# Kernel optimization log

Hardware: AMD Instinct MI355X
Metric: run time of the kernel (lower is better)

The kernel has to match this reference:

```python
import jax, jax.numpy as jnp
import numpy as np

NUM_HEADS = 16
NUM_KV_HEADS = 4
HEAD_DIM = 128
HIDDEN = 2048
SEQ = 2048
BATCH = 2
Q_PER_GROUP = NUM_HEADS // NUM_KV_HEADS          # 4
GROUP_SIZE = (Q_PER_GROUP + 2) * HEAD_DIM        # 768
TOTAL_PROJ = NUM_KV_HEADS * GROUP_SIZE           # 3072


def setup_inputs() -> dict:
    key = jax.random.key(0)
    k1, k2, k3 = jax.random.split(key, 3)
    x = jax.random.normal(k1, (SEQ, BATCH, HIDDEN), dtype=jnp.float32)
    w_qkv = jax.random.normal(k2, (TOTAL_PROJ, HIDDEN), dtype=jnp.float32) * 0.02
    w_proj = jax.random.normal(k3, (HIDDEN, NUM_HEADS * HEAD_DIM), dtype=jnp.float32) * 0.02
    return {"x": x, "w_qkv": w_qkv, "w_proj": w_proj}


def reference(x, w_qkv, w_proj):
    s, b, _ = x.shape
    # fused QKV projection (GQA-packed layout: per kv-group [q...q, k, v])
    qkv = jnp.einsum('sbh,ph->sbp', x, w_qkv)                       # [s,b,3072]
    qkv = qkv.reshape(s, b, NUM_KV_HEADS, GROUP_SIZE)
    q = qkv[..., :Q_PER_GROUP * HEAD_DIM].reshape(s, b, NUM_HEADS, HEAD_DIM)
    k = qkv[..., Q_PER_GROUP * HEAD_DIM:(Q_PER_GROUP + 1) * HEAD_DIM]  # [s,b,kvh,d]
    v = qkv[..., (Q_PER_GROUP + 1) * HEAD_DIM:]                        # [s,b,kvh,d]
    # to [b, heads, s, d]; expand kv heads over query groups (GQA)
    q = q.transpose(1, 2, 0, 3)
    k = jnp.repeat(k.transpose(1, 2, 0, 3), Q_PER_GROUP, axis=1)
    v = jnp.repeat(v.transpose(1, 2, 0, 3), Q_PER_GROUP, axis=1)
    scale = 1.0 / jnp.sqrt(jnp.asarray(HEAD_DIM, dtype=x.dtype))
    scores = jnp.einsum('bhsd,bhtd->bhst', q, k) * scale           # [b,h,s,s]
    attn = jax.nn.softmax(scores, axis=-1)
    out = jnp.einsum('bhst,bhtd->bhsd', attn, v)                    # [b,h,s,d]
    out = out.transpose(2, 0, 1, 3).reshape(s, b, NUM_HEADS * HEAD_DIM)
    return jnp.einsum('sbe,he->sbh', out, w_proj)                   # [s,b,hidden]
```

## Files before the change

### kernel.cpp

```cpp
#include <hip/hip_runtime.h>
#include <hip/hip_bf16.h>

typedef __bf16 bf16;
typedef __bf16 bf16x8 __attribute__((ext_vector_type(8)));
typedef __bf16 bf16x4v __attribute__((ext_vector_type(4)));
typedef float  f32x4  __attribute__((ext_vector_type(4)));
typedef float  f32x16 __attribute__((ext_vector_type(16)));

#define SEQL  2048
#define BATCH 2
#define HID   2048
#define NH    16
#define NKVH  4
#define HD    128
#define NPROJ 3072
#define MROWS 4096

__device__ __forceinline__ void gload16(const void* src, void* dst) {
  __builtin_amdgcn_global_load_lds(
      (__attribute__((address_space(1))) void*)src,
      (__attribute__((address_space(3))) void*)dst, 16, 0, 0);
}

__device__ __forceinline__ int swz128(int off) { return off ^ (((off >> 7) & 7) << 4); }
__device__ __forceinline__ int swz256(int off) { return off ^ (((off >> 8) & 7) << 4); }

__device__ __forceinline__ unsigned cvtpk_bf16(float lo, float hi) {
  unsigned r;
  asm("v_cvt_pk_bf16_f32 %0, %1, %2" : "=v"(r) : "v"(lo), "v"(hi));
  return r;
}
__device__ __forceinline__ void permswap32(unsigned& a, unsigned& b) {
  asm volatile("v_permlane32_swap_b32 %0, %1" : "+v"(a), "+v"(b));
}

__global__ __launch_bounds__(256) void cvt_kernel(
    const float* __restrict__ x, const float* __restrict__ wq, const float* __restrict__ wp,
    bf16* __restrict__ xo, bf16* __restrict__ wqo, bf16* __restrict__ wpo) {
  const int NXQ  = (MROWS * HID) / 4;
  const int NWQQ = (NPROJ * HID) / 4;
  const int NWPQ = (HID * HID) / 4;
  const int total = NXQ + NWQQ + NWPQ;
  for (int i = blockIdx.x * blockDim.x + threadIdx.x; i < total; i += gridDim.x * blockDim.x) {
    const float4* src; bf16* dst; int j;
    if (i < NXQ)            { src = (const float4*)x;  dst = xo;  j = i; }
    else if (i < NXQ + NWQQ){ src = (const float4*)wq; dst = wqo; j = i - NXQ; }
    else                    { src = (const float4*)wp; dst = wpo; j = i - NXQ - NWQQ; }
    float4 v = src[j];
    bf16x4v o;
    o[0] = (bf16)v.x; o[1] = (bf16)v.y; o[2] = (bf16)v.z; o[3] = (bf16)v.w;
    *(bf16x4v*)(dst + (size_t)j * 4) = o;
  }
}

__global__ __launch_bounds__(256, 3) void qkv_gemm(
    const bf16* __restrict__ A, const bf16* __restrict__ B,
    bf16* __restrict__ Qo, bf16* __restrict__ Ko, bf16* __restrict__ Vt) {
  __shared__ char lds[32768];
  const int tid = threadIdx.x, l = tid & 63, w = tid >> 6;
  const int lin = blockIdx.x + 24 * blockIdx.y;
  const int swz = (lin & 7) * 96 + (lin >> 3);
  const int bx = swz % 24, by = swz / 24;
  const int r0 = by * 128, p0 = bx * 128;
  const int wr = w >> 1, wc = w & 1;

  f32x4 acc[4][4];
  const f32x4 fzero = {0.f, 0.f, 0.f, 0.f};
#pragma unroll
  for (int m = 0; m < 4; m++)
#pragma unroll
    for (int n = 0; n < 4; n++) acc[m][n] = fzero;

  for (int kt = 0; kt < HID / 64; ++kt) {
    const int k0 = kt * 64;
    __syncthreads();
#pragma unroll
    for (int q = 0; q < 4; q++) {
      const int doff = (w * 4 + q) * 1024 + l * 16;
      const int row = doff >> 7;
      const int chv = ((doff >> 4) & 7) ^ (row & 7);
      gload16((const char*)A + ((size_t)(r0 + row) * HID + k0) * 2 + chv * 16,
              lds + (w * 4 + q) * 1024);
      gload16((const char*)B + ((size_t)(p0 + row) * HID + k0) * 2 + chv * 16,
              lds + 16384 + (w * 4 + q) * 1024);
    }
    __syncthreads();
    bf16x8 af[4][2], bfr[4][2];
#pragma unroll
    for (int m = 0; m < 4; m++)
#pragma unroll
      for (int kk = 0; kk < 2; kk++) {
        int off = (wr * 64 + m * 16 + (l & 15)) * 128 + kk * 64 + (l >> 4) * 16;
        af[m][kk] = *(const bf16x8*)(lds + swz128(off));
      }
#pragma unroll
    for (int n = 0; n < 4; n++)
#pragma unroll
      for (int kk = 0; kk < 2; kk++) {
        int off = (wc * 64 + n * 16 + (l & 15)) * 128 + kk * 64 + (l >> 4) * 16;
        bfr[n][kk] = *(const bf16x8*)(lds + 16384 + swz128(off));
      }
#pragma unroll
    for (int kk = 0; kk < 2; kk++)
#pragma unroll
      for (int m = 0; m < 4; m++)
#pragma unroll
        for (int n = 0; n < 4; n++)
          acc[m][n] = __builtin_amdgcn_mfma_f32_16x16x32_bf16(af[m][kk], bfr[n][kk], acc[m][n], 0, 0, 0);
  }

  const int seg = (p0 % 768) / 128;
  const int g = p0 / 768;
#pragma unroll
  for (int m = 0; m < 4; m++) {
    const int rbase = r0 + wr * 64 + m * 16 + ((l >> 4) << 2);
#pragma unroll
    for (int n = 0; n < 4; n++) {
      const int c = wc * 64 + n * 16 + (l & 15);
#pragma unroll
      for (int rg = 0; rg < 4; ++rg) {
        const int r = rbase + rg;
        const int s = r >> 1, b = r & 1;
        const bf16 val = (bf16)acc[m][n][rg];
        if (seg < 4) {
          const int h = g * 4 + seg;
          Qo[(((size_t)(b * 16 + h)) * 2048 + s) * 128 + c] = val;
        } else if (seg == 4) {
          Ko[(((size_t)(b * 4 + g)) * 2048 + s) * 128 + c] = val;
        } else {
          Vt[(((size_t)(b * 4 + g)) * 128 + c) * 2048 + s] = val;
        }
      }
    }
  }
}

template<int BASE>
__device__ __forceinline__ void attn_tile(
    char* lds, const bf16x8* qf, const int* ka, const int* va,
    f32x16* oacc, f32x16& lacc, float& m_r, bf16x8 ones) {
  const float CEXP = 0.08838834764831845f * 1.44269504088896340f;
  const float THR_RAW = 8.0f / CEXP;
  const f32x16 z16 = {};

  f32x16 sT0 = z16, sT1 = z16;
  __builtin_amdgcn_s_setprio(1);
#pragma unroll
  for (int s = 0; s < 8; s++) {
    bf16x8 kf = *(const bf16x8*)(lds + BASE + ka[s]);
    sT0 = __builtin_amdgcn_mfma_f32_32x32x16_bf16(kf, qf[s], sT0, 0, 0, 0);
  }
#pragma unroll
  for (int s = 0; s < 8; s++) {
    bf16x8 kf = *(const bf16x8*)(lds + BASE + ka[8 + s]);
    sT1 = __builtin_amdgcn_mfma_f32_32x32x16_bf16(kf, qf[s], sT1, 0, 0, 0);
  }
  __builtin_amdgcn_s_setprio(0);

  float tmx[16];
#pragma unroll
  for (int i = 0; i < 16; i++) tmx[i] = fmaxf(sT0[i], sT1[i]);
#pragma unroll
  for (int st = 8; st >= 1; st >>= 1)
#pragma unroll
    for (int i = 0; i < 8; i++)
      if (i < st) tmx[i] = fmaxf(tmx[i], tmx[i + st]);
  float mx = tmx[0];
  mx = fmaxf(mx, __shfl_xor(mx, 32));

  if (!__all(mx <= m_r + THR_RAW)) {
    const float mnew = fmaxf(m_r, mx);
    const float corr = exp2f((m_r - mnew) * CEXP);
    m_r = mnew;
#pragma unroll
    for (int d = 0; d < 4; d++)
#pragma unroll
      for (int i = 0; i < 16; i++) oacc[d][i] *= corr;
#pragma unroll
    for (int i = 0; i < 16; i++) lacc[i] *= corr;
  }

#pragma unroll
  for (int i = 0; i < 16; i++) sT0[i] = exp2f((sT0[i] - m_r) * CEXP);
#pragma unroll
  for (int i = 0; i < 16; i++) sT1[i] = exp2f((sT1[i] - m_r) * CEXP);

  unsigned c0[8], c1[8];
#pragma unroll
  for (int i = 0; i < 8; i++) c0[i] = cvtpk_bf16(sT0[2 * i], sT0[2 * i + 1]);
#pragma unroll
  for (int i = 0; i < 8; i++) c1[i] = cvtpk_bf16(sT1[2 * i], sT1[2 * i + 1]);
  permswap32(c0[0], c0[2]); permswap32(c0[1], c0[3]);
  permswap32(c0[4], c0[6]); permswap32(c0[5], c0[7]);
  permswap32(c1[0], c1[2]); permswap32(c1[1], c1[3]);
  permswap32(c1[4], c1[6]); permswap32(c1[5], c1[7]);

  __builtin_amdgcn_s_setprio(1);
#pragma unroll
  for (int ks = 0; ks < 4; ks++) {
    union { unsigned u[4]; bf16x8 v; } pb;
    const unsigned* cs = (ks < 2) ? c0 : c1;
#pragma unroll
    for (int i = 0; i < 4; i++) pb.u[i] = cs[(ks & 1) * 4 + i];
    lacc = __builtin_amdgcn_mfma_f32_32x32x16_bf16(ones, pb.v, lacc, 0, 0, 0);
#pragma unroll
    for (int dblk = 0; dblk < 4; dblk++) {
      bf16x8 vf = *(const bf16x8*)(lds + BASE + 16384 + va[ks * 4 + dblk]);
      oacc[dblk] = __builtin_amdgcn_mfma_f32_32x32x16_bf16(vf, pb.v, oacc[dblk], 0, 0, 0);
    }
  }
  __builtin_amdgcn_s_setprio(0);
}

__global__ __launch_bounds__(256, 2) void attn_kernel(
    const bf16* __restrict__ Q, const bf16* __restrict__ K, const bf16* __restrict__ V,
    bf16* __restrict__ O) {
  __shared__ char lds[65536];
  const int tid = threadIdx.x, l = tid & 63, w = tid >> 6;
  const int l31 = l & 31, h2 = l >> 5;
  const int lin = blockIdx.x + (blockIdx.y << 4);
  const int swzb = (lin & 7) * 64 + (lin >> 3);
  const int qt = swzb & 15, bh = swzb >> 4;
  const int b = bh >> 4, head = bh & 15, g = head >> 2;

  const int q0 = qt * 128 + w * 32;

  bf16x8 qf[8];
  {
    const bf16* qbase = Q + (((size_t)(b * 16 + head)) * 2048 + q0 + l31) * 128 + h2 * 8;
#pragma unroll
    for (int s = 0; s < 8; s++) qf[s] = *(const bf16x8*)(qbase + s * 16);
  }

  int ka[16], va[16];
#pragma unroll
  for (int tsub = 0; tsub < 2; tsub++)
#pragma unroll
    for (int s = 0; s < 8; s++)
      ka[tsub * 8 + s] = swz256((tsub * 32 + l31) * 256 + s * 32 + h2 * 16);
#pragma unroll
  for (int ks = 0; ks < 4; ks++)
#pragma unroll
    for (int dblk = 0; dblk < 4; dblk++)
      va[ks * 4 + dblk] = swz128((dblk * 32 + l31) * 128 + ks * 32 + h2 * 16);

  int kso[4], vso[4];
#pragma unroll
  for (int q = 0; q < 4; q++) {
    const int off = (q * 4 + w) * 1024 + l * 16;
    kso[q] = swz256(off);
    const int rowv = off >> 7;
    const int chv = ((off >> 4) & 7) ^ (rowv & 7);
    vso[q] = rowv * 4096 + chv * 16;
  }

  bf16x8 ones;
#pragma unroll
  for (int i = 0; i < 8; i++) ones[i] = (bf16)1.0f;

  const f32x16 z16 = {};
  f32x16 oacc[4];
#pragma unroll
  for (int d = 0; d < 4; d++) oacc[d] = z16;
  f32x16 lacc = z16;
  float m_r = -1e30f;

  const char* kbase = (const char*)(K + ((size_t)(b * 4 + g)) * 2048 * 128);
  const char* vbase = (const char*)(V + ((size_t)(b * 4 + g)) * 128 * 2048);

  auto stage = [&](int t0, int B) {
#pragma unroll
    for (int q = 0; q < 4; q++) {
      gload16(kbase + (size_t)t0 * 256 + kso[q], lds + B + (q * 4 + w) * 1024);
      gload16(vbase + (size_t)t0 * 2 + vso[q], lds + B + 16384 + (q * 4 + w) * 1024);
    }
  };

  stage(0, 0);
  __syncthreads();

  for (int t0 = 0; t0 < SEQL; t0 += 128) {
    stage(t0 + 64, 32768);
    attn_tile<0>(lds, qf, ka, va, oacc, lacc, m_r, ones);
    __syncthreads();
    if (t0 + 128 < SEQL) stage(t0 + 128, 0);
    attn_tile<32768>(lds, qf, ka, va, oacc, lacc, m_r, ones);
    __syncthreads();
  }

  const float inv = 1.0f / lacc[0];
  const size_t rowo = ((size_t)(q0 + l31) * 2 + b) * 2048 + (size_t)head * 128;
#pragma unroll
  for (int dblk = 0; dblk < 4; dblk++)
#pragma unroll
    for (int g4 = 0; g4 < 4; g4++) {
      bf16x4v ov;
#pragma unroll
      for (int e = 0; e < 4; e++) ov[e] = (bf16)(oacc[dblk][g4 * 4 + e] * inv);
      *(bf16x4v*)(O + rowo + dblk * 32 + g4 * 8 + h2 * 4) = ov;
    }
}

__global__ __launch_bounds__(256, 2) void proj_gemm(
    const bf16* __restrict__ A, const bf16* __restrict__ B, float* __restrict__ C) {
  __shared__ char lds[32768];
  const int tid = threadIdx.x, l = tid & 63, w = tid >> 6;
  const int lin = blockIdx.x + (blockIdx.y << 4);
  const int swz = (lin & 7) * 64 + (lin >> 3);
  const int bx = swz & 15, by = swz >> 4;
  const int r0 = by * 128, p0 = bx * 128;
  const int wr = w >> 1, wc = w & 1;

  f32x4 acc[4][4];
  const f32x4 fzero = {0.f, 0.f, 0.f, 0.f};
#pragma unroll
  for (int m = 0; m < 4; m++)
#pragma unroll
    for (int n = 0; n < 4; n++) acc[m][n] = fzero;

  for (int kt = 0; kt < HID / 64; ++kt) {
    const int k0 = kt * 64;
    __syncthreads();
#pragma unroll
    for (int q = 0; q < 4; q++) {
      const int doff = (w * 4 + q) * 1024 + l * 16;
      const int row = doff >> 7;
      const int chv = ((doff >> 4) & 7) ^ (row & 7);
      gload16((const char*)A + ((size_t)(r0 + row) * HID + k0) * 2 + chv * 16,
              lds + (w * 4 + q) * 1024);
      gload16((const char*)B + ((size_t)(p0 + row) * HID + k0) * 2 + chv * 16,
              lds + 16384 + (w * 4 + q) * 1024);
    }
    __syncthreads();
    bf16x8 af[4][2], bfr[4][2];
#pragma unroll
    for (int m = 0; m < 4; m++)
#pragma unroll
      for (int kk = 0; kk < 2; kk++) {
        int off = (wr * 64 + m * 16 + (l & 15)) * 128 + kk * 64 + (l >> 4) * 16;
        af[m][kk] = *(const bf16x8*)(lds + swz128(off));
      }
#pragma unroll
    for (int n = 0; n < 4; n++)
#pragma unroll
      for (int kk = 0; kk < 2; kk++) {
        int off = (wc * 64 + n * 16 + (l & 15)) * 128 + kk * 64 + (l >> 4) * 16;
        bfr[n][kk] = *(const bf16x8*)(lds + 16384 + swz128(off));
      }
#pragma unroll
    for (int kk = 0; kk < 2; kk++)
#pragma unroll
      for (int m = 0; m < 4; m++)
#pragma unroll
        for (int n = 0; n < 4; n++)
          acc[m][n] = __builtin_amdgcn_mfma_f32_16x16x32_bf16(af[m][kk], bfr[n][kk], acc[m][n], 0, 0, 0);
  }
#pragma unroll
  for (int m = 0; m < 4; m++) {
    const int rbase = r0 + wr * 64 + m * 16 + ((l >> 4) << 2);
#pragma unroll
    for (int n = 0; n < 4; n++) {
      const int c = p0 + wc * 64 + n * 16 + (l & 15);
#pragma unroll
      for (int rg = 0; rg < 4; ++rg)
        C[(size_t)(rbase + rg) * HID + c] = acc[m][n][rg];
    }
  }
}

extern "C" void kernel_launch(void* const* d_in, const int* in_sizes, int n_in,
                              void* d_out, int out_size, void* d_ws, size_t ws_size,
                              hipStream_t stream) {
  const float* x  = (const float*)d_in[0];
  const float* wq = (const float*)d_in[1];
  const float* wp = (const float*)d_in[2];
  float* out = (float*)d_out;
  char* ws = (char*)d_ws;

  size_t off = 0;
  bf16* xb  = (bf16*)(ws + off); off += (size_t)MROWS * HID * 2;
  bf16* wqb = (bf16*)(ws + off); off += (size_t)NPROJ * HID * 2;
  bf16* wpb = (bf16*)(ws + off); off += (size_t)HID * HID * 2;
  bf16* Qb  = (bf16*)(ws + off); off += (size_t)2 * 16 * 2048 * 128 * 2;
  bf16* Kb  = (bf16*)(ws + off); off += (size_t)2 * 4 * 2048 * 128 * 2;
  bf16* Vb  = (bf16*)(ws + off); off += (size_t)2 * 4 * 128 * 2048 * 2;
  bf16* Ob  = xb;

  cvt_kernel<<<2048, 256, 0, stream>>>(x, wq, wp, xb, wqb, wpb);
  qkv_gemm<<<dim3(24, 32), 256, 0, stream>>>(xb, wqb, Qb, Kb, Vb);
  attn_kernel<<<dim3(16, 32), 256, 0, stream>>>(Qb, Kb, Vb, Ob);
  proj_gemm<<<dim3(16, 32), 256, 0, stream>>>(Ob, wpb, out);
}
```

Measured before the change: 212.8 us.

## Process two query sub-tiles per wave in attention and fold softmax scale into Q

Each attention wave now handles 64 query rows as two 32-row sub-tiles, so every K/V fragment read from LDS is reused for two MFMA chains. The grid is halved and launch bounds drop to one block per CU to leave room for the doubled accumulators. The softmax scale times log2(e) is folded into Q at the QKV GEMM epilogue, which removes a multiply per score element in the exp path. This trades occupancy and register pressure for less LDS traffic per MFMA and fewer K/V reloads, and the grid of 256 blocks may leave some CUs idle.

```diff
diff --git a/kernel.cpp b/kernel.cpp
--- a/kernel.cpp
+++ b/kernel.cpp
@@ -15,6 +15,8 @@
 #define HD    128
 #define NPROJ 3072
 #define MROWS 4096
+
+#define QSCALE (0.08838834764831845f * 1.44269504088896340f)
 
 __device__ __forceinline__ void gload16(const void* src, void* dst) {
   __builtin_amdgcn_global_load_lds(
@@ -121,42 +123,24 @@
       for (int rg = 0; rg < 4; ++rg) {
         const int r = rbase + rg;
         const int s = r >> 1, b = r & 1;
-        const bf16 val = (bf16)acc[m][n][rg];
         if (seg < 4) {
           const int h = g * 4 + seg;
-          Qo[(((size_t)(b * 16 + h)) * 2048 + s) * 128 + c] = val;
+          Qo[(((size_t)(b * 16 + h)) * 2048 + s) * 128 + c] = (bf16)(acc[m][n][rg] * QSCALE);
         } else if (seg == 4) {
-          Ko[(((size_t)(b * 4 + g)) * 2048 + s) * 128 + c] = val;
+          Ko[(((size_t)(b * 4 + g)) * 2048 + s) * 128 + c] = (bf16)acc[m][n][rg];
         } else {
-          Vt[(((size_t)(b * 4 + g)) * 128 + c) * 2048 + s] = val;
+          Vt[(((size_t)(b * 4 + g)) * 128 + c) * 2048 + s] = (bf16)acc[m][n][rg];
         }
       }
     }
   }
 }
 
-template<int BASE>
-__device__ __forceinline__ void attn_tile(
-    char* lds, const bf16x8* qf, const int* ka, const int* va,
-    f32x16* oacc, f32x16& lacc, float& m_r, bf16x8 ones) {
-  const float CEXP = 0.08838834764831845f * 1.44269504088896340f;
-  const float THR_RAW = 8.0f / CEXP;
-  const f32x16 z16 = {};
-
-  f32x16 sT0 = z16, sT1 = z16;
-  __builtin_amdgcn_s_setprio(1);
-#pragma unroll
-  for (int s = 0; s < 8; s++) {
-    bf16x8 kf = *(const bf16x8*)(lds + BASE + ka[s]);
-    sT0 = __builtin_amdgcn_mfma_f32_32x32x16_bf16(kf, qf[s], sT0, 0, 0, 0);
-  }
-#pragma unroll
-  for (int s = 0; s < 8; s++) {
-    bf16x8 kf = *(const bf16x8*)(lds + BASE + ka[8 + s]);
-    sT1 = __builtin_amdgcn_mfma_f32_32x32x16_bf16(kf, qf[s], sT1, 0, 0, 0);
-  }
-  __builtin_amdgcn_s_setprio(0);
-
+#define THR_LOG2 11.5415603f
+
+__device__ __forceinline__ void softmax_pack(
+    f32x16& sT0, f32x16& sT1, f32x16* oacc, f32x16& lacc, float& m_r,
+    unsigned* c0, unsigned* c1) {
   float tmx[16];
 #pragma unroll
   for (int i = 0; i < 16; i++) tmx[i] = fmaxf(sT0[i], sT1[i]);
@@ -168,9 +152,9 @@
   float mx = tmx[0];
   mx = fmaxf(mx, __shfl_xor(mx, 32));
 
-  if (!__all(mx <= m_r + THR_RAW)) {
+  if (!__all(mx <= m_r + THR_LOG2)) {
     const float mnew = fmaxf(m_r, mx);
-    const float corr = exp2f((m_r - mnew) * CEXP);
+    const float corr = exp2f(m_r - mnew);
     m_r = mnew;
 #pragma unroll
     for (int d = 0; d < 4; d++)
@@ -181,11 +165,10 @@
   }
 
 #pragma unroll
-  for (int i = 0; i < 16; i++) sT0[i] = exp2f((sT0[i] - m_r) * CEXP);
-#pragma unroll
-  for (int i = 0; i < 16; i++) sT1[i] = exp2f((sT1[i] - m_r) * CEXP);
-
-  unsigned c0[8], c1[8];
+  for (int i = 0; i < 16; i++) sT0[i] = exp2f(sT0[i] - m_r);
+#pragma unroll
+  for (int i = 0; i < 16; i++) sT1[i] = exp2f(sT1[i] - m_r);
+
 #pragma unroll
   for (int i = 0; i < 8; i++) c0[i] = cvtpk_bf16(sT0[2 * i], sT0[2 * i + 1]);
 #pragma unroll
@@ -194,42 +177,74 @@
   permswap32(c0[4], c0[6]); permswap32(c0[5], c0[7]);
   permswap32(c1[0], c1[2]); permswap32(c1[1], c1[3]);
   permswap32(c1[4], c1[6]); permswap32(c1[5], c1[7]);
-
+}
+
+template<int BASE>
+__device__ __forceinline__ void attn_tile(
+    char* lds, const bf16x8* qfA, const bf16x8* qfB, const int* ka, const int* va,
+    f32x16* oA, f32x16* oB, f32x16& lA, f32x16& lB, float& mA, float& mB, bf16x8 ones) {
+  const f32x16 z16 = {};
+
+  f32x16 sA0 = z16, sA1 = z16, sB0 = z16, sB1 = z16;
   __builtin_amdgcn_s_setprio(1);
 #pragma unroll
+  for (int s = 0; s < 8; s++) {
+    bf16x8 kf = *(const bf16x8*)(lds + BASE + ka[s]);
+    sA0 = __builtin_amdgcn_mfma_f32_32x32x16_bf16(kf, qfA[s], sA0, 0, 0, 0);
+    sB0 = __builtin_amdgcn_mfma_f32_32x32x16_bf16(kf, qfB[s], sB0, 0, 0, 0);
+  }
+#pragma unroll
+  for (int s = 0; s < 8; s++) {
+    bf16x8 kf = *(const bf16x8*)(lds + BASE + ka[8 + s]);
+    sA1 = __builtin_amdgcn_mfma_f32_32x32x16_bf16(kf, qfA[s], sA1, 0, 0, 0);
+    sB1 = __builtin_amdgcn_mfma_f32_32x32x16_bf16(kf, qfB[s], sB1, 0, 0, 0);
+  }
+  __builtin_amdgcn_s_setprio(0);
+
+  unsigned cA0[8], cA1[8], cB0[8], cB1[8];
+  softmax_pack(sA0, sA1, oA, lA, mA, cA0, cA1);
+  softmax_pack(sB0, sB1, oB, lB, mB, cB0, cB1);
+
+  __builtin_amdgcn_s_setprio(1);
+#pragma unroll
   for (int ks = 0; ks < 4; ks++) {
-    union { unsigned u[4]; bf16x8 v; } pb;
-    const unsigned* cs = (ks < 2) ? c0 : c1;
-#pragma unroll
-    for (int i = 0; i < 4; i++) pb.u[i] = cs[(ks & 1) * 4 + i];
-    lacc = __builtin_amdgcn_mfma_f32_32x32x16_bf16(ones, pb.v, lacc, 0, 0, 0);
+    union { unsigned u[4]; bf16x8 v; } pA, pB;
+    const unsigned* csA = (ks < 2) ? cA0 : cA1;
+    const unsigned* csB = (ks < 2) ? cB0 : cB1;
+#pragma unroll
+    for (int i = 0; i < 4; i++) { pA.u[i] = csA[(ks & 1) * 4 + i]; pB.u[i] = csB[(ks & 1) * 4 + i]; }
+    lA = __builtin_amdgcn_mfma_f32_32x32x16_bf16(ones, pA.v, lA, 0, 0, 0);
+    lB = __builtin_amdgcn_mfma_f32_32x32x16_bf16(ones, pB.v, lB, 0, 0, 0);
 #pragma unroll
     for (int dblk = 0; dblk < 4; dblk++) {
       bf16x8 vf = *(const bf16x8*)(lds + BASE + 16384 + va[ks * 4 + dblk]);
-      oacc[dblk] = __builtin_amdgcn_mfma_f32_32x32x16_bf16(vf, pb.v, oacc[dblk], 0, 0, 0);
+      oA[dblk] = __builtin_amdgcn_mfma_f32_32x32x16_bf16(vf, pA.v, oA[dblk], 0, 0, 0);
+      oB[dblk] = __builtin_amdgcn_mfma_f32_32x32x16_bf16(vf, pB.v, oB[dblk], 0, 0, 0);
     }
   }
   __builtin_amdgcn_s_setprio(0);
 }
 
-__global__ __launch_bounds__(256, 2) void attn_kernel(
+__global__ __launch_bounds__(256, 1) void attn_kernel(
     const bf16* __restrict__ Q, const bf16* __restrict__ K, const bf16* __restrict__ V,
     bf16* __restrict__ O) {
   __shared__ char lds[65536];
   const int tid = threadIdx.x, l = tid & 63, w = tid >> 6;
   const int l31 = l & 31, h2 = l >> 5;
-  const int lin = blockIdx.x + (blockIdx.y << 4);
-  const int swzb = (lin & 7) * 64 + (lin >> 3);
-  const int qt = swzb & 15, bh = swzb >> 4;
+  const int lin = blockIdx.x + (blockIdx.y << 3);
+  const int swzb = (lin & 7) * 32 + (lin >> 3);
+  const int qt = swzb & 7, bh = swzb >> 3;
   const int b = bh >> 4, head = bh & 15, g = head >> 2;
 
-  const int q0 = qt * 128 + w * 32;
-
-  bf16x8 qf[8];
+  const int q0 = qt * 256 + w * 64;
+
+  bf16x8 qfA[8], qfB[8];
   {
     const bf16* qbase = Q + (((size_t)(b * 16 + head)) * 2048 + q0 + l31) * 128 + h2 * 8;
 #pragma unroll
-    for (int s = 0; s < 8; s++) qf[s] = *(const bf16x8*)(qbase + s * 16);
+    for (int s = 0; s < 8; s++) qfA[s] = *(const bf16x8*)(qbase + s * 16);
+#pragma unroll
+    for (int s = 0; s < 8; s++) qfB[s] = *(const bf16x8*)(qbase + 32 * 128 + s * 16);
   }
 
   int ka[16], va[16];
@@ -259,11 +274,11 @@
   for (int i = 0; i < 8; i++) ones[i] = (bf16)1.0f;
 
   const f32x16 z16 = {};
-  f32x16 oacc[4];
-#pragma unroll
-  for (int d = 0; d < 4; d++) oacc[d] = z16;
-  f32x16 lacc = z16;
-  float m_r = -1e30f;
+  f32x16 oA[4], oB[4];
+#pragma unroll
+  for (int d = 0; d < 4; d++) { oA[d] = z16; oB[d] = z16; }
+  f32x16 lA = z16, lB = z16;
+  float mA = -1e30f, mB = -1e30f;
 
   const char* kbase = (const char*)(K + ((size_t)(b * 4 + g)) * 2048 * 128);
   const char* vbase = (const char*)(V + ((size_t)(b * 4 + g)) * 128 * 2048);
@@ -281,24 +296,39 @@
 
   for (int t0 = 0; t0 < SEQL; t0 += 128) {
     stage(t0 + 64, 32768);
-    attn_tile<0>(lds, qf, ka, va, oacc, lacc, m_r, ones);
+    attn_tile<0>(lds, qfA, qfB, ka, va, oA, oB, lA, lB, mA, mB, ones);
     __syncthreads();
     if (t0 + 128 < SEQL) stage(t0 + 128, 0);
-    attn_tile<32768>(lds, qf, ka, va, oacc, lacc, m_r, ones);
-    __syncthreads();
-  }
-
-  const float inv = 1.0f / lacc[0];
-  const size_t rowo = ((size_t)(q0 + l31) * 2 + b) * 2048 + (size_t)head * 128;
-#pragma unroll
-  for (int dblk = 0; dblk < 4; dblk++)
-#pragma unroll
-    for (int g4 = 0; g4 < 4; g4++) {
-      bf16x4v ov;
-#pragma unroll
-      for (int e = 0; e < 4; e++) ov[e] = (bf16)(oacc[dblk][g4 * 4 + e] * inv);
-      *(bf16x4v*)(O + rowo + dblk * 32 + g4 * 8 + h2 * 4) = ov;
-    }
+    attn_tile<32768>(lds, qfA, qfB, ka, va, oA, oB, lA, lB, mA, mB, ones);
+    __syncthreads();
+  }
+
+  {
+    const float inv = 1.0f / lA[0];
+    const size_t rowo = ((size_t)(q0 + l31) * 2 + b) * 2048 + (size_t)head * 128;
+#pragma unroll
+    for (int dblk = 0; dblk < 4; dblk++)
+#pragma unroll
+      for (int g4 = 0; g4 < 4; g4++) {
+        bf16x4v ov;
+#pragma unroll
+        for (int e = 0; e < 4; e++) ov[e] = (bf16)(oA[dblk][g4 * 4 + e] * inv);
+        *(bf16x4v*)(O + rowo + dblk * 32 + g4 * 8 + h2 * 4) = ov;
+      }
+  }
+  {
+    const float inv = 1.0f / lB[0];
+    const size_t rowo = ((size_t)(q0 + 32 + l31) * 2 + b) * 2048 + (size_t)head * 128;
+#pragma unroll
+    for (int dblk = 0; dblk < 4; dblk++)
+#pragma unroll
+      for (int g4 = 0; g4 < 4; g4++) {
+        bf16x4v ov;
+#pragma unroll
+        for (int e = 0; e < 4; e++) ov[e] = (bf16)(oB[dblk][g4 * 4 + e] * inv);
+        *(bf16x4v*)(O + rowo + dblk * 32 + g4 * 8 + h2 * 4) = ov;
+      }
+  }
 }
 
 __global__ __launch_bounds__(256, 2) void proj_gemm(
@@ -388,6 +418,6 @@
 
   cvt_kernel<<<2048, 256, 0, stream>>>(x, wq, wp, xb, wqb, wpb);
   qkv_gemm<<<dim3(24, 32), 256, 0, stream>>>(xb, wqb, Qb, Kb, Vb);
-  attn_kernel<<<dim3(16, 32), 256, 0, stream>>>(Qb, Kb, Vb, Ob);
+  attn_kernel<<<dim3(8, 32), 256, 0, stream>>>(Qb, Kb, Vb, Ob);
   proj_gemm<<<dim3(16, 32), 256, 0, stream>>>(Ob, wpb, out);
 }
```

Result: slower. 287.4 us (+35.1%).
